# Optimization experiments

Measured on AMD Instinct MI355X. Metric: run time of the kernel, lower is better.

Reference implementation:

```python
import jax, jax.numpy as jnp
from jax import lax
import numpy as np

DN = ('NCHW', 'OIHW', 'NCHW')

def conv2d(x, w, b, stride=1, padding=1):
    out = lax.conv_general_dilated(
        x, w, window_strides=(stride, stride),
        padding=[(padding, padding), (padding, padding)],
        dimension_numbers=DN)
    return out + b[None, :, None, None]

def maxpool2d(x, k=2, s=2):
    return lax.reduce_window(x, -jnp.inf, lax.max,
                             window_dimensions=(1, 1, k, k),
                             window_strides=(1, 1, s, s),
                             padding='VALID')

def setup_inputs() -> dict:
    key = jax.random.key(0)
    ks = jax.random.split(key, 9)
    B = 4096
    x = jax.random.normal(ks[0], (B, 3, 32, 32), dtype=jnp.float32)
    # weights initialized like torch.randn(...) * 0.1, biases zeros
    w1 = jax.random.normal(ks[1], (16, 3, 3, 3), dtype=jnp.float32) * 0.1
    b1 = jnp.zeros((16,), jnp.float32)
    w2 = jax.random.normal(ks[2], (32, 16, 3, 3), dtype=jnp.float32) * 0.1
    b2 = jnp.zeros((32,), jnp.float32)
    w3 = jax.random.normal(ks[3], (64, 32, 3, 3), dtype=jnp.float32) * 0.1
    b3 = jnp.zeros((64,), jnp.float32)
    # fc: Linear(64*4*4, 10); kaiming-uniform-ish init
    fan_in = 64 * 4 * 4
    bound = 1.0 / np.sqrt(fan_in)
    fc_w = jax.random.uniform(ks[4], (10, fan_in), jnp.float32, -bound, bound)
    fc_b = jax.random.uniform(ks[5], (10,), jnp.float32, -bound, bound)
    return {"x": x, "w1": w1, "b1": b1, "w2": w2, "b2": b2,
            "w3": w3, "b3": b3, "fc_w": fc_w, "fc_b": fc_b}

def reference(x, w1, b1, w2, b2, w3, b3, fc_w, fc_b):
    h = maxpool2d(jax.nn.relu(conv2d(x, w1, b1)))   # [B,16,16,16]
    h = maxpool2d(jax.nn.relu(conv2d(h, w2, b2)))   # [B,32,8,8]
    h = maxpool2d(jax.nn.relu(conv2d(h, w3, b3)))   # [B,64,4,4]
    h = h.reshape(h.shape[0], -1)                    # [B,1024]
    # dropout is identity in eval mode
    return h @ fc_w.T + fc_b
```

## Files before the change

kernel.cpp:

```cpp
#include <hip/hip_runtime.h>

typedef float f32x4 __attribute__((ext_vector_type(4)));
typedef float f32x16v __attribute__((ext_vector_type(16)));
typedef __bf16 bf16x4 __attribute__((ext_vector_type(4)));
typedef __bf16 bf16x8 __attribute__((ext_vector_type(8)));

#define B2P_OFF 0
#define B3P_OFF 9216
#define C1P_OFF 46080

__global__ __launch_bounds__(256) void pack_weights(
    const float* __restrict__ w1, const float* __restrict__ w2,
    const float* __restrict__ w3, __bf16* __restrict__ wsb) {
  int i = blockIdx.x * 256 + threadIdx.x;
  if (i < 9216) {
    int f = i >> 9, r = i & 511;
    int l = r >> 3, j = r & 7;
    int t = f >> 1, p = f & 1;
    int ky = t / 3, kx = t % 3;
    int oc = l & 31, ic = ((l >> 5) << 3) + j;
    float v = w2[oc * 144 + ic * 9 + ky * 3 + kx];
    __bf16 hi = (__bf16)v;
    wsb[B2P_OFF + i] = p ? (__bf16)(v - (float)hi) : hi;
  } else if (i < 9216 + 36864) {
    int q = i - 9216;
    int f = q >> 9, r = q & 511;
    int l = r >> 3, j = r & 7;
    int t = f >> 3, nt = (f >> 1) & 3, p = f & 1;
    int ky = t / 3, kx = t % 3;
    int oc = nt * 16 + (l & 15), ic = ((l >> 4) << 3) + j;
    float v = w3[oc * 288 + ic * 9 + ky * 3 + kx];
    __bf16 hi = (__bf16)v;
    wsb[B3P_OFF + q] = p ? (__bf16)(v - (float)hi) : hi;
  } else if (i < 9216 + 36864 + 1024) {
    int q = i - (9216 + 36864);
    int f = q >> 9, r = q & 511;
    int l = r >> 3, j = r & 7;
    int oc = l & 15, kg = l >> 4;
    int half = j >> 2, ic = j & 3;
    float v = 0.f;
    if (ic < 3) {
      if (f == 0) {
        if (kg < 3)            v = w1[oc * 27 + ic * 9 + kg * 3 + half];
        else if (half == 0)    v = w1[oc * 27 + ic * 9 + 0 * 3 + 2];
      } else {
        if (half == 0 && kg < 2) v = w1[oc * 27 + ic * 9 + (kg + 1) * 3 + 2];
      }
    }
    wsb[C1P_OFF + q] = (__bf16)v;
  }
}

__global__ __launch_bounds__(256, 4) void cnn_fused(
    const float* __restrict__ x, const __bf16* __restrict__ wsb,
    const float* __restrict__ b1, const float* __restrict__ b2,
    const float* __restrict__ b3,
    const float* __restrict__ fcw, const float* __restrict__ fcb,
    float* __restrict__ out) {
  __shared__ __align__(16) unsigned char smem[25408];
  __bf16* s_img = (__bf16*)smem;
  __bf16* s2b   = (__bf16*)(smem + 9280);
  __bf16* s3b   = (__bf16*)smem;
  float*  h3s   = (float*)(smem + 9280);

  const __bf16* b2p = wsb + B2P_OFF;
  const __bf16* b3p = wsb + B3P_OFF;
  const __bf16* c1p = wsb + C1P_OFF;

  const int tid = threadIdx.x;
  const int img = blockIdx.x;
  const int w = tid >> 6, lane = tid & 63;

  if (tid < 132) {
    int row, col;
    if (tid < 34)       { row = 0;        col = tid; }
    else if (tid < 68)  { row = 33;       col = tid - 34; }
    else if (tid < 100) { row = tid - 67; col = 0; }
    else                { row = tid - 99; col = 33; }
    *(unsigned long long*)&s_img[(row * 34 + col) * 4] = 0ull;
  } else if (tid >= 248 && tid < 252) {
    *(unsigned long long*)&s_img[4624 + (tid - 248) * 4] = 0ull;
  }
  {
    const float* xg = x + img * 3072;
    const int r = tid * 4;
    const int y = r >> 5, xx = r & 31;
    const f32x4 c0 = *(const f32x4*)&xg[r];
    const f32x4 c1 = *(const f32x4*)&xg[r + 1024];
    const f32x4 c2 = *(const f32x4*)&xg[r + 2048];
    bf16x4 pk[4];
    #pragma unroll
    for (int k = 0; k < 4; ++k) {
      pk[k].x = (__bf16)c0[k];
      pk[k].y = (__bf16)c1[k];
      pk[k].z = (__bf16)c2[k];
      pk[k].w = (__bf16)0.f;
    }
    const int base = ((y + 1) * 34 + (xx + 1)) * 4;
    __builtin_memcpy(&s_img[base],     &pk[0], 16);
    __builtin_memcpy(&s_img[base + 8], &pk[2], 16);
  }
  const bf16x8 B1h = *(const bf16x8*)(c1p + lane * 8);
  const bf16x8 B2h = *(const bf16x8*)(c1p + 512 + lane * 8);
  __syncthreads();

  float pooled[16];
  {
    const int xm = lane & 15, kg = lane >> 4;
    const int d1r = (kg == 3) ? 0 : kg;
    const int d1c = (kg == 3) ? 2 : 0;
    const int d2r = (kg == 0) ? 1 : 2;
    const int dd1 = d1r * 34 + d1c;
    const int dd2 = d2r * 34 + 2;
    #pragma unroll
    for (int p = 0; p < 4; ++p) {
      f32x4 acc[2][2];
      #pragma unroll
      for (int ys = 0; ys < 2; ++ys)
        #pragma unroll
        for (int xh = 0; xh < 2; ++xh)
          #pragma unroll
          for (int r = 0; r < 4; ++r) acc[ys][xh][r] = 0.f;
      #pragma unroll
      for (int ys = 0; ys < 2; ++ys) {
        const int yqg = w * 8 + p * 2 + ys;
        #pragma unroll
        for (int xh = 0; xh < 2; ++xh) {
          const int cb = yqg * 34 + xh * 16 + xm;
          bf16x8 A1, A2;
          __builtin_memcpy(&A1, &s_img[(cb + dd1) * 4], 16);
          __builtin_memcpy(&A2, &s_img[(cb + dd2) * 4], 16);
          acc[ys][xh] = __builtin_amdgcn_mfma_f32_16x16x32_bf16(A1, B1h, acc[ys][xh], 0, 0, 0);
          acc[ys][xh] = __builtin_amdgcn_mfma_f32_16x16x32_bf16(A2, B2h, acc[ys][xh], 0, 0, 0);
        }
      }
      #pragma unroll
      for (int xh = 0; xh < 2; ++xh)
        #pragma unroll
        for (int xp2 = 0; xp2 < 2; ++xp2) {
          const float v0 = fmaxf(acc[0][xh][xp2 * 2], acc[0][xh][xp2 * 2 + 1]);
          const float v1 = fmaxf(acc[1][xh][xp2 * 2], acc[1][xh][xp2 * 2 + 1]);
          pooled[p * 4 + xh * 2 + xp2] = fmaxf(v0, v1);
        }
    }
  }

  if (tid < 68) {
    int row, col;
    if (tid < 18)      { row = 0;       col = tid; }
    else if (tid < 36) { row = 17;      col = tid - 18; }
    else if (tid < 52) { row = tid - 35; col = 0; }
    else               { row = tid - 51; col = 17; }
    unsigned long long* p = (unsigned long long*)&s2b[row * 448 + col * 24];
    p[0] = 0ull; p[1] = 0ull; p[2] = 0ull; p[3] = 0ull;
  }
  {
    const int oc = lane & 15, quad = lane >> 4;
    const float bias = b1[oc];
    #pragma unroll
    for (int p = 0; p < 4; ++p)
      #pragma unroll
      for (int xh = 0; xh < 2; ++xh)
        #pragma unroll
        for (int xp2 = 0; xp2 < 2; ++xp2) {
          const float v = fmaxf(pooled[p * 4 + xh * 2 + xp2] + bias, 0.f);
          const int py = w * 4 + p, px = xh * 8 + quad * 2 + xp2;
          s2b[(py + 1) * 448 + (px + 1) * 24 + oc] = (__bf16)v;
        }
  }
  bf16x8 Bf[9];
  #pragma unroll
  for (int t = 0; t < 9; ++t)
    Bf[t] = *(const bf16x8*)(b2p + (t * 2) * 512 + lane * 8);
  __syncthreads();

  float pooled2[8];
  {
    const unsigned short* s2 = (const unsigned short*)s2b;
    const int xm = lane & 15, yoff = (lane >> 4) & 1, kh = lane >> 5;
    #pragma unroll
    for (int i2 = 0; i2 < 2; ++i2) {
      f32x16v acc;
      #pragma unroll
      for (int r = 0; r < 16; ++r) acc[r] = 0.f;
      const int rbase = (4 * w + yoff + 2 * i2) * 448;
      #pragma unroll
      for (int t = 0; t < 9; ++t) {
        const int ky = t / 3, kx = t % 3;
        const int ro = rbase + ky * 448 + (xm + kx) * 24 + kh * 8;
        bf16x8 ah = *(const bf16x8*)&s2[ro];
        acc = __builtin_amdgcn_mfma_f32_32x32x16_bf16(ah, Bf[t], acc, 0, 0, 0);
      }
      #pragma unroll
      for (int bq = 0; bq < 2; ++bq)
        #pragma unroll
        for (int rq = 0; rq < 2; ++rq) {
          const int r0 = bq * 4 + rq * 2;
          pooled2[i2 * 4 + bq * 2 + rq] =
              fmaxf(fmaxf(acc[r0], acc[r0 + 1]), fmaxf(acc[r0 + 8], acc[r0 + 9]));
        }
    }
  }

  if (tid < 36) {
    int row, col;
    if (tid < 10)      { row = 0;       col = tid; }
    else if (tid < 20) { row = 9;       col = tid - 10; }
    else if (tid < 28) { row = tid - 19; col = 0; }
    else               { row = tid - 27; col = 9; }
    unsigned long long* p = (unsigned long long*)&s3b[row * 448 + col * 40];
    #pragma unroll
    for (int u = 0; u < 8; ++u) p[u] = 0ull;
  }
  {
    const int oc = lane & 31, hh = lane >> 5;
    const float bias = b2[oc];
    #pragma unroll
    for (int i2 = 0; i2 < 2; ++i2)
      #pragma unroll
      for (int bq = 0; bq < 2; ++bq)
        #pragma unroll
        for (int rq = 0; rq < 2; ++rq) {
          const float v = fmaxf(pooled2[i2 * 4 + bq * 2 + rq] + bias, 0.f);
          const int py = 2 * w + i2, px = 2 * hh + 4 * bq + rq;
          s3b[(py + 1) * 448 + (px + 1) * 40 + oc] = (__bf16)v;
        }
  }
  __syncthreads();

  {
    const unsigned short* s3 = (const unsigned short*)s3b;
    const int nt = w;
    bf16x8 Bt[9];
    #pragma unroll
    for (int t = 0; t < 9; ++t)
      Bt[t] = *(const bf16x8*)(b3p + (t * 8 + nt * 2) * 512 + lane * 8);
    const int m = lane & 15, quad = lane >> 4;
    const int xm = m & 7, yoff = m >> 3;
    f32x4 acc[4];
    #pragma unroll
    for (int mt = 0; mt < 4; ++mt)
      #pragma unroll
      for (int r = 0; r < 4; ++r) acc[mt][r] = 0.f;
    #pragma unroll
    for (int t = 0; t < 9; ++t) {
      const int ky = t / 3, kx = t % 3;
      #pragma unroll
      for (int mt = 0; mt < 4; ++mt) {
        const int ro = (2 * mt + yoff + ky) * 448 + (xm + kx) * 40 + quad * 8;
        bf16x8 ah = *(const bf16x8*)&s3[ro];
        acc[mt] = __builtin_amdgcn_mfma_f32_16x16x32_bf16(ah, Bt[t], acc[mt], 0, 0, 0);
      }
    }
    const int ocl = lane & 15;
    #pragma unroll
    for (int mt = 0; mt < 4; ++mt) {
      float p0 = fmaxf(acc[mt][0], acc[mt][1]);
      float p1 = fmaxf(acc[mt][2], acc[mt][3]);
      p0 = fmaxf(p0, __shfl_xor(p0, 32, 64));
      p1 = fmaxf(p1, __shfl_xor(p1, 32, 64));
      if (quad < 2) {
        const int oc = nt * 16 + ocl;
        const float bias = b3[oc];
        const int base = oc * 20 + mt * 4 + (quad & 1) * 2;
        h3s[base]     = fmaxf(p0 + bias, 0.f);
        h3s[base + 1] = fmaxf(p1 + bias, 0.f);
      }
    }
  }
  __syncthreads();

  {
    f32x4 hv[4];
    #pragma unroll
    for (int k = 0; k < 4; ++k) hv[k] = *(const f32x4*)&h3s[lane * 20 + k * 4];
    for (int j = w; j < 10; j += 4) {
      const f32x4* fw4 = (const f32x4*)&fcw[j * 1024 + lane * 16];
      float dot = 0.f;
      #pragma unroll
      for (int k = 0; k < 4; ++k) {
        const f32x4 fv = fw4[k];
        dot = fmaf(hv[k][0], fv[0], dot);
        dot = fmaf(hv[k][1], fv[1], dot);
        dot = fmaf(hv[k][2], fv[2], dot);
        dot = fmaf(hv[k][3], fv[3], dot);
      }
      #pragma unroll
      for (int s = 32; s > 0; s >>= 1) dot += __shfl_xor(dot, s, 64);
      if (lane == 0) out[img * 10 + j] = dot + fcb[j];
    }
  }
}

extern "C" void kernel_launch(void* const* d_in, const int* in_sizes, int n_in,
                              void* d_out, int out_size, void* d_ws, size_t ws_size,
                              hipStream_t stream) {
  const float* x   = (const float*)d_in[0];
  const float* w1  = (const float*)d_in[1];
  const float* b1  = (const float*)d_in[2];
  const float* w2  = (const float*)d_in[3];
  const float* b2  = (const float*)d_in[4];
  const float* w3  = (const float*)d_in[5];
  const float* b3  = (const float*)d_in[6];
  const float* fcw = (const float*)d_in[7];
  const float* fcb = (const float*)d_in[8];
  __bf16* wsb = (__bf16*)d_ws;
  float* out = (float*)d_out;

  hipLaunchKernelGGL(pack_weights, dim3(184), dim3(256), 0, stream, w1, w2, w3, wsb);
  hipLaunchKernelGGL(cnn_fused, dim3(4096), dim3(256), 0, stream,
                     x, wsb, b1, b2, b3, fcw, fcb, out);
}
```

Baseline: 127.4 us.

## Switch conv3 to 32x32x16 MFMA tiles with 2x2 warp split

Conv3 moves from 16x16x32 MFMA tiles (one wave per 16-channel slice over four M tiles) to 32x32x16 MFMA, with each wave covering a 32-pixel by 32-channel tile. The weight packing is rewritten to match the new B-fragment layout and packs fewer conv3 weight elements. Pooling now happens inside a lane's accumulator registers instead of through a cross-lane shuffle. The intent is fewer MFMA issues and A-operand LDS reads per wave, at the cost of more weight registers per wave (18 B fragments instead of 9).

```diff
diff --git a/kernel.cpp b/kernel.cpp
--- a/kernel.cpp
+++ b/kernel.cpp
@@ -22,18 +22,17 @@
     float v = w2[oc * 144 + ic * 9 + ky * 3 + kx];
     __bf16 hi = (__bf16)v;
     wsb[B2P_OFF + i] = p ? (__bf16)(v - (float)hi) : hi;
-  } else if (i < 9216 + 36864) {
+  } else if (i < 9216 + 18432) {
     int q = i - 9216;
     int f = q >> 9, r = q & 511;
     int l = r >> 3, j = r & 7;
-    int t = f >> 3, nt = (f >> 1) & 3, p = f & 1;
+    int t = f >> 2, h = (f >> 1) & 1, nt = f & 1;
     int ky = t / 3, kx = t % 3;
-    int oc = nt * 16 + (l & 15), ic = ((l >> 4) << 3) + j;
-    float v = w3[oc * 288 + ic * 9 + ky * 3 + kx];
-    __bf16 hi = (__bf16)v;
-    wsb[B3P_OFF + q] = p ? (__bf16)(v - (float)hi) : hi;
-  } else if (i < 9216 + 36864 + 1024) {
-    int q = i - (9216 + 36864);
+    int oc = nt * 32 + (l & 31);
+    int ic = h * 16 + ((l >> 5) << 3) + j;
+    wsb[B3P_OFF + q] = (__bf16)w3[oc * 288 + ic * 9 + ky * 3 + kx];
+  } else if (i >= 46080 && i < 47104) {
+    int q = i - 46080;
     int f = q >> 9, r = q & 511;
     int l = r >> 3, j = r & 7;
     int oc = l & 15, kg = l >> 4;
@@ -230,43 +229,39 @@
 
   {
     const unsigned short* s3 = (const unsigned short*)s3b;
-    const int nt = w;
-    bf16x8 Bt[9];
+    const int mtile = w >> 1, ntile = w & 1;
+    bf16x8 Bt[18];
     #pragma unroll
     for (int t = 0; t < 9; ++t)
-      Bt[t] = *(const bf16x8*)(b3p + (t * 8 + nt * 2) * 512 + lane * 8);
-    const int m = lane & 15, quad = lane >> 4;
-    const int xm = m & 7, yoff = m >> 3;
-    f32x4 acc[4];
-    #pragma unroll
-    for (int mt = 0; mt < 4; ++mt)
-      #pragma unroll
-      for (int r = 0; r < 4; ++r) acc[mt][r] = 0.f;
+      #pragma unroll
+      for (int h = 0; h < 2; ++h)
+        Bt[t * 2 + h] = *(const bf16x8*)(b3p + (t * 4 + h * 2 + ntile) * 512 + lane * 8);
+    const int m = lane & 31, half = lane >> 5;
+    const int py = m >> 3, px = m & 7;
+    f32x16v acc;
+    #pragma unroll
+    for (int r = 0; r < 16; ++r) acc[r] = 0.f;
     #pragma unroll
     for (int t = 0; t < 9; ++t) {
       const int ky = t / 3, kx = t % 3;
-      #pragma unroll
-      for (int mt = 0; mt < 4; ++mt) {
-        const int ro = (2 * mt + yoff + ky) * 448 + (xm + kx) * 40 + quad * 8;
-        bf16x8 ah = *(const bf16x8*)&s3[ro];
-        acc[mt] = __builtin_amdgcn_mfma_f32_16x16x32_bf16(ah, Bt[t], acc[mt], 0, 0, 0);
-      }
-    }
-    const int ocl = lane & 15;
-    #pragma unroll
-    for (int mt = 0; mt < 4; ++mt) {
-      float p0 = fmaxf(acc[mt][0], acc[mt][1]);
-      float p1 = fmaxf(acc[mt][2], acc[mt][3]);
-      p0 = fmaxf(p0, __shfl_xor(p0, 32, 64));
-      p1 = fmaxf(p1, __shfl_xor(p1, 32, 64));
-      if (quad < 2) {
-        const int oc = nt * 16 + ocl;
-        const float bias = b3[oc];
-        const int base = oc * 20 + mt * 4 + (quad & 1) * 2;
-        h3s[base]     = fmaxf(p0 + bias, 0.f);
-        h3s[base + 1] = fmaxf(p1 + bias, 0.f);
-      }
-    }
+      const int ro = (mtile * 4 + py + ky) * 448 + (px + kx) * 40 + half * 8;
+      bf16x8 a0 = *(const bf16x8*)&s3[ro];
+      bf16x8 a1 = *(const bf16x8*)&s3[ro + 16];
+      acc = __builtin_amdgcn_mfma_f32_32x32x16_bf16(a0, Bt[t * 2 + 0], acc, 0, 0, 0);
+      acc = __builtin_amdgcn_mfma_f32_32x32x16_bf16(a1, Bt[t * 2 + 1], acc, 0, 0, 0);
+    }
+    const int oc = ntile * 32 + (lane & 31);
+    const float bias = b3[oc];
+    #pragma unroll
+    for (int i = 0; i < 2; ++i)
+      #pragma unroll
+      for (int jq = 0; jq < 2; ++jq) {
+        const int r0 = 8 * i + 2 * jq;
+        const float v = fmaxf(fmaxf(acc[r0], acc[r0 + 1]),
+                              fmaxf(acc[r0 + 4], acc[r0 + 5]));
+        const int gy = mtile * 2 + i, gx = 2 * half + jq;
+        h3s[oc * 20 + gy * 4 + gx] = fmaxf(v + bias, 0.f);
+      }
   }
   __syncthreads();
 
```

Result: faster. 124.7 us (-2.1%).
